# Kernel tuning notes

Measured on AMD Instinct MI355X. Metric: run time of the kernel, lower is better.

The kernel has to match this reference:

```python
import jax, jax.numpy as jnp
import numpy as np

H = W = 64
C = 256
NUM_HEADS = 8

# Static index maps from AbsolutePositionalWeighting.__init__
_center_h = (H - 1) // 2
_center_w = (W - 1) // 2
_gi, _gj = np.meshgrid(np.arange(H), np.arange(W), indexing='ij')
_dx = _gi - _center_h
_dy = _gj - _center_w
DH = max(int(np.abs(_dx).max()), _center_h)
DW = max(int(np.abs(_dy).max()), _center_w)
DX_IDX = jnp.asarray(_dx + DH)  # (H, W)
DY_IDX = jnp.asarray(_dy + DW)  # (H, W)


def setup_inputs() -> dict:
    key = jax.random.key(0)
    ks = jax.random.split(key, 6)
    B, N = 16, H * W
    x1 = jax.random.normal(ks[0], (B, N, C), dtype=jnp.float32)
    x2 = jax.random.normal(ks[1], (B, N, C), dtype=jnp.float32)
    x3 = jax.random.normal(ks[2], (B, N, C), dtype=jnp.float32)
    pos_weights = 0.1 * jax.random.normal(ks[3], (2 * DH + 1, 2 * DW + 1, C), dtype=jnp.float32)
    lepe_w = 0.1 * jax.random.normal(ks[4], (C, 1, 3, 3), dtype=jnp.float32)  # depthwise OIHW
    lepe_b = 0.01 * jax.random.normal(ks[5], (C,), dtype=jnp.float32)
    return {"x1": x1, "x2": x2, "x3": x3, "pos_weights": pos_weights,
            "lepe_w": lepe_w, "lepe_b": lepe_b}


def reference(x1, x2, x3, pos_weights, lepe_w, lepe_b):
    b, n, c = x1.shape
    nh, hd = NUM_HEADS, c // NUM_HEADS

    q = jax.nn.elu(x1) + 1.0
    k = jax.nn.elu(x2) + 1.0
    v = x3

    # Positional gating: sigmoid(pos_weights gathered at per-pixel offsets) -> (N, C)
    pw = jax.nn.sigmoid(pos_weights[DX_IDX, DY_IDX, :]).reshape(n, c)
    q_rope = q * pw[None]  # (b, n, c)
    k_rope = k * pw[None]

    # Split heads: (b, n, nh, hd)
    q4 = q.reshape(b, n, nh, hd)
    k4 = k.reshape(b, n, nh, hd)
    v4 = v.reshape(b, n, nh, hd)
    qr4 = q_rope.reshape(b, n, nh, hd)
    kr4 = k_rope.reshape(b, n, nh, hd)

    # Normalizer z = 1 / (q . mean_n(k) + eps)
    k_mean = k4.mean(axis=1)  # (b, nh, hd)
    z = 1.0 / (jnp.einsum('bnhd,bhd->bnh', q4, k_mean) + 1e-6)

    # Linear attention: kv = (k_rope/sqrt(n))^T (v/sqrt(n)); out = q_rope @ kv * z
    kv = jnp.einsum('bnhd,bnhe->bhde', kr4, v4) / n  # (b, nh, hd, hd)
    attn = jnp.einsum('bnhd,bhde->bnhe', qr4, kv) * z[..., None]
    attn = attn.reshape(b, n, c)

    # LePE: depthwise 3x3 conv on v image (NCHW)
    v_img = v.reshape(b, H, W, c).transpose(0, 3, 1, 2)
    lepe = jax.lax.conv_general_dilated(
        v_img, lepe_w, window_strides=(1, 1), padding='SAME',
        feature_group_count=c,
        dimension_numbers=('NCHW', 'OIHW', 'NCHW'))
    lepe = lepe + lepe_b[None, :, None, None]
    lepe = lepe.transpose(0, 2, 3, 1).reshape(b, n, c)

    return attn + lepe
```

## Files before the change

kernel.cpp:

```cpp
#include <hip/hip_runtime.h>

#define BB 16
#define HIMG 64
#define WIMG 64
#define CC 256
#define NHEAD 8
#define HD 32
#define NN 4096
#define PWD 65
#define PADC 264

typedef short bf16x8 __attribute__((ext_vector_type(8)));
typedef float f32x4 __attribute__((ext_vector_type(4)));

__device__ __forceinline__ float elu1(float x) {
    return x > 0.0f ? x + 1.0f : __expf(x);
}
__device__ __forceinline__ float sigm(float x) {
    return 1.0f / (1.0f + __expf(-x));
}
__device__ __forceinline__ unsigned short f2bf(float f) {
    union { float f; unsigned int u; } v; v.f = f;
    unsigned int r = v.u + 0x7FFFu + ((v.u >> 16) & 1u);
    return (unsigned short)(r >> 16);
}

__global__ __launch_bounds__(256) void k0_pw(
    const float* __restrict__ posw, float* __restrict__ pw)
{
    const int gid = blockIdx.x * 256 + threadIdx.x;
    const int n = gid >> 6;
    const int p = gid & 63;
    const int ii = n >> 6, jj = n & 63;
    const float4 v = *(const float4*)(posw + (size_t)((ii + 1) * PWD + (jj + 1)) * CC + p * 4);
    float4 r;
    r.x = sigm(v.x); r.y = sigm(v.y); r.z = sigm(v.z); r.w = sigm(v.w);
    *(float4*)(pw + (size_t)n * CC + p * 4) = r;
}

__global__ __launch_bounds__(256) void k1_partial(
    const float* __restrict__ x2, const float* __restrict__ x3,
    const float* __restrict__ pw, float* __restrict__ pkv,
    float* __restrict__ pksum, int nchl, int rows)
{
    const int blk   = blockIdx.x;
    const int b     = blk >> nchl;
    const int chunk = blk & ((1 << nchl) - 1);
    const int n0    = chunk * rows;
    const int t     = threadIdx.x;
    const int p     = t & 127;
    const int pp    = p - 64;
    const int rbase = t >> 7;

    const int h   = t >> 5;
    const int idx = t & 31;
    const int dt  = idx & 7;
    const int et  = idx >> 3;

    __shared__ float kr_lds[2][4][CC];
    __shared__ float v_lds[2][4][CC];
    __shared__ float ksum_lds[2][CC];

    float acc[4][8];
#pragma unroll
    for (int a = 0; a < 4; ++a)
#pragma unroll
        for (int e = 0; e < 8; ++e) acc[a][e] = 0.0f;
    float ks0 = 0.f, ks1 = 0.f, ks2 = 0.f, ks3 = 0.f;

    const float* x2b = x2 + (size_t)b * NN * CC;
    const float* x3b = x3 + (size_t)b * NN * CC;

    const int nstep = rows >> 2;
    float4 kx[2], pv[2], vx[2];

    {
        const int r0 = n0;
        if (p < 64) {
#pragma unroll
            for (int it = 0; it < 2; ++it) {
                const int n = r0 + rbase + 2 * it;
                kx[it] = *(const float4*)(x2b + (size_t)n * CC + p * 4);
            }
#pragma unroll
            for (int it = 0; it < 2; ++it) {
                const int n = r0 + rbase + 2 * it;
                pv[it] = *(const float4*)(pw + (size_t)n * CC + p * 4);
            }
        } else {
#pragma unroll
            for (int it = 0; it < 2; ++it) {
                const int n = r0 + rbase + 2 * it;
                vx[it] = *(const float4*)(x3b + (size_t)n * CC + pp * 4);
            }
        }
    }

    int buf = 0;
    for (int s = 0; s < nstep; ++s) {
        if (p < 64) {
#pragma unroll
            for (int it = 0; it < 2; ++it) {
                const int row = rbase + 2 * it;
                float4 kk;
                kk.x = elu1(kx[it].x); kk.y = elu1(kx[it].y);
                kk.z = elu1(kx[it].z); kk.w = elu1(kx[it].w);
                float4 kr;
                kr.x = kk.x * pv[it].x; kr.y = kk.y * pv[it].y;
                kr.z = kk.z * pv[it].z; kr.w = kk.w * pv[it].w;
                *(float4*)(&kr_lds[buf][row][p * 4]) = kr;
                ks0 += kk.x; ks1 += kk.y; ks2 += kk.z; ks3 += kk.w;
            }
        } else {
#pragma unroll
            for (int it = 0; it < 2; ++it)
                *(float4*)(&v_lds[buf][rbase + 2 * it][pp * 4]) = vx[it];
        }
        __syncthreads();
        if (s + 1 < nstep) {
            const int r0 = n0 + (s + 1) * 4;
            if (p < 64) {
#pragma unroll
                for (int it = 0; it < 2; ++it) {
                    const int n = r0 + rbase + 2 * it;
                    kx[it] = *(const float4*)(x2b + (size_t)n * CC + p * 4);
                }
#pragma unroll
                for (int it = 0; it < 2; ++it) {
                    const int n = r0 + rbase + 2 * it;
                    pv[it] = *(const float4*)(pw + (size_t)n * CC + p * 4);
                }
            } else {
#pragma unroll
                for (int it = 0; it < 2; ++it) {
                    const int n = r0 + rbase + 2 * it;
                    vx[it] = *(const float4*)(x3b + (size_t)n * CC + pp * 4);
                }
            }
        }
#pragma unroll
        for (int r = 0; r < 4; ++r) {
            const float4 k4 = *(const float4*)(&kr_lds[buf][r][h * HD + dt * 4]);
            const float4 va = *(const float4*)(&v_lds[buf][r][h * HD + et * 8]);
            const float4 vb = *(const float4*)(&v_lds[buf][r][h * HD + et * 8 + 4]);
            const float kd[4] = {k4.x, k4.y, k4.z, k4.w};
            const float ve[8] = {va.x, va.y, va.z, va.w, vb.x, vb.y, vb.z, vb.w};
#pragma unroll
            for (int a = 0; a < 4; ++a)
#pragma unroll
                for (int e = 0; e < 8; ++e)
                    acc[a][e] = fmaf(kd[a], ve[e], acc[a][e]);
        }
        buf ^= 1;
    }

    if (p < 64) {
        ksum_lds[rbase][p * 4 + 0] = ks0;
        ksum_lds[rbase][p * 4 + 1] = ks1;
        ksum_lds[rbase][p * 4 + 2] = ks2;
        ksum_lds[rbase][p * 4 + 3] = ks3;
    }
    __syncthreads();
    pksum[(size_t)blk * CC + t] = ksum_lds[0][t] + ksum_lds[1][t];

    float* dst = pkv + (size_t)blk * (NHEAD * HD * HD);
#pragma unroll
    for (int a = 0; a < 4; ++a)
#pragma unroll
        for (int e = 0; e < 8; ++e)
            dst[h * (HD * HD) + (dt * 4 + a) * HD + (et * 8 + e)] = acc[a][e];
}

__global__ __launch_bounds__(256) void k2_reduce(
    const float* __restrict__ pkv, const float* __restrict__ pksum,
    unsigned short* __restrict__ kvbT, float* __restrict__ kmean, int nch)
{
    const int gid = blockIdx.x * 256 + threadIdx.x;
    const int b = gid >> 13;
    const int o = gid & 8191;
    float s = 0.f;
#pragma unroll 4
    for (int c = 0; c < nch; ++c)
        s += pkv[(size_t)(b * nch + c) * (NHEAD * HD * HD) + o];
    const int hh = o >> 10, d = (o >> 5) & 31, e = o & 31;
    kvbT[(((size_t)b * NHEAD + hh) * HD + e) * HD + d] = f2bf(s * (1.0f / NN));
    if (o < CC) {
        float ss = 0.f;
#pragma unroll 4
        for (int c = 0; c < nch; ++c)
            ss += pksum[(size_t)(b * nch + c) * CC + o];
        kmean[b * CC + o] = ss * (1.0f / NN);
    }
}

__global__ __launch_bounds__(256, 2) void k3_out(
    const float* __restrict__ x1, const float* __restrict__ x3,
    const float* __restrict__ pw, const unsigned short* __restrict__ kvbT,
    const float* __restrict__ kmean, const float* __restrict__ lw,
    const float* __restrict__ lb, float* __restrict__ out)
{
    const int blk  = blockIdx.x;
    const int b    = blk >> 8;
    const int irow = (blk >> 2) & 63;
    const int jq   = blk & 3;
    const int j0   = jq << 4;
    const int t    = threadIdx.x;

    __shared__ unsigned short qr_bf[16 * PADC];
    __shared__ float attn_lds[16][CC];

    float wreg[9];
#pragma unroll
    for (int q = 0; q < 9; ++q) wreg[q] = lw[t * 9 + q];
    const float bias = lb[t];

    {
        const int p    = t & 63;
        const int pixo = t >> 6;
        const float4 km4 = *(const float4*)(kmean + b * CC + p * 4);
        const float* x1b = x1 + ((size_t)b * NN + (size_t)irow * 64 + j0) * CC;
        const float* pwb = pw + ((size_t)irow * 64 + j0) * CC;
        float4 xv[4], pvv[4];
#pragma unroll
        for (int s = 0; s < 4; ++s)
            xv[s] = *(const float4*)(x1b + (size_t)(s * 4 + pixo) * CC + p * 4);
#pragma unroll
        for (int s = 0; s < 4; ++s)
            pvv[s] = *(const float4*)(pwb + (size_t)(s * 4 + pixo) * CC + p * 4);
#pragma unroll
        for (int s = 0; s < 4; ++s) {
            const int pix = s * 4 + pixo;
            float4 q4;
            q4.x = elu1(xv[s].x); q4.y = elu1(xv[s].y);
            q4.z = elu1(xv[s].z); q4.w = elu1(xv[s].w);
            float zp = q4.x * km4.x + q4.y * km4.y + q4.z * km4.z + q4.w * km4.w;
            zp += __shfl_xor(zp, 1);
            zp += __shfl_xor(zp, 2);
            zp += __shfl_xor(zp, 4);
            const float zin = 1.0f / (zp + 1e-6f);
            ushort4 u;
            u.x = f2bf(q4.x * pvv[s].x * zin);
            u.y = f2bf(q4.y * pvv[s].y * zin);
            u.z = f2bf(q4.z * pvv[s].z * zin);
            u.w = f2bf(q4.w * pvv[s].w * zin);
            *(ushort4*)(&qr_bf[pix * PADC + p * 4]) = u;
        }
    }

    const bool hasU = irow > 0, hasD = irow < 63;
    const float* rU = x3 + ((size_t)b * NN + (size_t)(irow - 1) * 64 + j0) * CC + t;
    const float* rM = x3 + ((size_t)b * NN + (size_t)irow * 64 + j0) * CC + t;
    const float* rD = x3 + ((size_t)b * NN + (size_t)(irow + 1) * 64 + j0) * CC + t;

    float cu[2][10], cm[2][10], cd[2][10];
#pragma unroll
    for (int tt = 0; tt < 2; ++tt)
#pragma unroll
        for (int q = 0; q < 10; ++q) {
            const int col = tt * 8 + q - 1;
            const int g   = j0 + col;
            const bool ok = (g >= 0) && (g < 64);
            const long off = (long)col * CC;
            cm[tt][q] = ok ? rM[off] : 0.f;
            cu[tt][q] = (ok && hasU) ? rU[off] : 0.f;
            cd[tt][q] = (ok && hasD) ? rD[off] : 0.f;
        }

    __syncthreads();

    {
        const int w  = t >> 6;
        const int l  = t & 63;
        const int lr = l & 15;
        const int lg = l >> 4;

        bf16x8 af0 = *(const bf16x8*)(&qr_bf[lr * PADC + (w * 2 + 0) * HD + lg * 8]);
        bf16x8 af1 = *(const bf16x8*)(&qr_bf[lr * PADC + (w * 2 + 1) * HD + lg * 8]);

        f32x4 acc[4];
#pragma unroll
        for (int ct = 0; ct < 4; ++ct) {
            const int head = w * 2 + (ct >> 1);
            const int cl   = (ct & 1) * 16 + lr;
            const bf16x8 bf = *(const bf16x8*)(kvbT +
                (((size_t)b * NHEAD + head) * HD + cl) * HD + lg * 8);
            f32x4 z4 = {0.f, 0.f, 0.f, 0.f};
            acc[ct] = __builtin_amdgcn_mfma_f32_16x16x32_bf16(
                (ct < 2) ? af0 : af1, bf, z4, 0, 0, 0);
        }
#pragma unroll
        for (int ct = 0; ct < 4; ++ct) {
            const int c = (w * 2 + (ct >> 1)) * HD + (ct & 1) * 16 + lr;
#pragma unroll
            for (int r = 0; r < 4; ++r)
                attn_lds[lg * 4 + r][c] = acc[ct][r];
        }
    }

    __syncthreads();

    float* ob = out + ((size_t)b * NN + (size_t)irow * 64 + j0) * CC + t;
#pragma unroll
    for (int tt = 0; tt < 2; ++tt) {
#pragma unroll
        for (int q = 0; q < 8; ++q) {
            const int jl = tt * 8 + q;
            float lepe = bias
                + wreg[0] * cu[tt][q] + wreg[1] * cu[tt][q + 1] + wreg[2] * cu[tt][q + 2]
                + wreg[3] * cm[tt][q] + wreg[4] * cm[tt][q + 1] + wreg[5] * cm[tt][q + 2]
                + wreg[6] * cd[tt][q] + wreg[7] * cd[tt][q + 1] + wreg[8] * cd[tt][q + 2];
            __builtin_nontemporal_store(attn_lds[jl][t] + lepe, ob + (long)jl * CC);
        }
    }
}

extern "C" void kernel_launch(void* const* d_in, const int* in_sizes, int n_in,
                              void* d_out, int out_size, void* d_ws, size_t ws_size,
                              hipStream_t stream) {
    const float* x1   = (const float*)d_in[0];
    const float* x2   = (const float*)d_in[1];
    const float* x3   = (const float*)d_in[2];
    const float* posw = (const float*)d_in[3];
    const float* lw   = (const float*)d_in[4];
    const float* lb   = (const float*)d_in[5];
    float* out = (float*)d_out;

    const size_t pw_sz = (size_t)NN * CC;
    const size_t need64 = (pw_sz + (size_t)16 * 64 * 8192 + (size_t)16 * 64 * 256 +
                           (size_t)16 * 256) * sizeof(float) +
                          (size_t)16 * 8192 * sizeof(unsigned short);
    const int nchl = (ws_size >= need64) ? 6 : 5;
    const int nch  = 1 << nchl;
    const int rows = NN >> nchl;

    float* pwb   = (float*)d_ws;
    float* pkv   = pwb + pw_sz;
    float* pksum = pkv + (size_t)16 * nch * 8192;
    float* kmean = pksum + (size_t)16 * nch * 256;
    unsigned short* kvbT = (unsigned short*)(kmean + (size_t)16 * 256);

    k0_pw<<<1024, 256, 0, stream>>>(posw, pwb);
    k1_partial<<<16 * nch, 256, 0, stream>>>(x2, x3, pwb, pkv, pksum, nchl, rows);
    k2_reduce<<<512, 256, 0, stream>>>(pkv, pksum, kvbT, kmean, nch);
    k3_out<<<BB * 256, 256, 0, stream>>>(x1, x3, pwb, kvbT, kmean, lw, lb, out);
}
```

Before: 100.7 us.

## Deepen k1 prefetch pipeline with uniform thread roles and 8-row steps

Rewrites the k1_partial main loop so every thread loads k, pw and v slices itself, replacing the old split between k-loading and v-loading halves. Each step now processes 8 rows instead of 4. Two register buffer sets keep global loads two steps ahead, with a single raw s_barrier per step. It also adds a min-blocks hint of 2 to launch_bounds. The aim is to keep more memory requests in flight and cut barrier overhead in this bandwidth-bound reduction, at the cost of more registers and LDS. It also assumes the step count is even.

```diff
diff --git a/kernel.cpp b/kernel.cpp
--- a/kernel.cpp
+++ b/kernel.cpp
@@ -38,7 +38,54 @@
     *(float4*)(pw + (size_t)n * CC + p * 4) = r;
 }
 
-__global__ __launch_bounds__(256) void k1_partial(
+
+#define K1_ISSUE(sS, kxS, pvS, vxS)                                          \
+    do {                                                                      \
+        const int r0_ = n0 + (sS) * 8;                                        \
+        const int na_ = r0_ + w, nb_ = r0_ + w + 4;                           \
+        kxS[0] = *(const float4*)(x2b + (size_t)na_ * CC + slot * 4);         \
+        kxS[1] = *(const float4*)(x2b + (size_t)nb_ * CC + slot * 4);         \
+        pvS[0] = *(const float4*)(pw  + (size_t)na_ * CC + slot * 4);         \
+        pvS[1] = *(const float4*)(pw  + (size_t)nb_ * CC + slot * 4);         \
+        vxS[0] = *(const float4*)(x3b + (size_t)na_ * CC + slot * 4);         \
+        vxS[1] = *(const float4*)(x3b + (size_t)nb_ * CC + slot * 4);         \
+    } while (0)
+
+#define K1_STEP(sS, kxS, pvS, vxS, bufS)                                      \
+    do {                                                                      \
+        _Pragma("unroll")                                                     \
+        for (int rp_ = 0; rp_ < 2; ++rp_) {                                   \
+            const int row_ = w + rp_ * 4;                                     \
+            float4 kk_;                                                       \
+            kk_.x = elu1(kxS[rp_].x); kk_.y = elu1(kxS[rp_].y);               \
+            kk_.z = elu1(kxS[rp_].z); kk_.w = elu1(kxS[rp_].w);               \
+            ks0 += kk_.x; ks1 += kk_.y; ks2 += kk_.z; ks3 += kk_.w;           \
+            float4 kr_;                                                       \
+            kr_.x = kk_.x * pvS[rp_].x; kr_.y = kk_.y * pvS[rp_].y;           \
+            kr_.z = kk_.z * pvS[rp_].z; kr_.w = kk_.w * pvS[rp_].w;           \
+            *(float4*)(&kr_lds[bufS][row_][slot * 4]) = kr_;                  \
+            *(float4*)(&v_lds[bufS][row_][slot * 4]) = vxS[rp_];              \
+        }                                                                     \
+        asm volatile("s_waitcnt lgkmcnt(0)" ::: "memory");                    \
+        __builtin_amdgcn_s_barrier();                                         \
+        if ((sS) + 2 < nstep) K1_ISSUE((sS) + 2, kxS, pvS, vxS);              \
+        _Pragma("unroll")                                                     \
+        for (int r_ = 0; r_ < 8; ++r_) {                                      \
+            const float4 k4_ = *(const float4*)(&kr_lds[bufS][r_][h * HD + dt * 4]);   \
+            const float4 va_ = *(const float4*)(&v_lds[bufS][r_][h * HD + et * 8]);    \
+            const float4 vb_ = *(const float4*)(&v_lds[bufS][r_][h * HD + et * 8 + 4]);\
+            const float kd_[4] = {k4_.x, k4_.y, k4_.z, k4_.w};                \
+            const float ve_[8] = {va_.x, va_.y, va_.z, va_.w,                 \
+                                  vb_.x, vb_.y, vb_.z, vb_.w};                \
+            _Pragma("unroll")                                                 \
+            for (int a_ = 0; a_ < 4; ++a_)                                    \
+                _Pragma("unroll")                                             \
+                for (int e_ = 0; e_ < 8; ++e_)                                \
+                    acc[a_][e_] = fmaf(kd_[a_], ve_[e_], acc[a_][e_]);        \
+        }                                                                     \
+    } while (0)
+
+__global__ __launch_bounds__(256, 2) void k1_partial(
     const float* __restrict__ x2, const float* __restrict__ x3,
     const float* __restrict__ pw, float* __restrict__ pkv,
     float* __restrict__ pksum, int nchl, int rows)
@@ -48,18 +95,17 @@
     const int chunk = blk & ((1 << nchl) - 1);
     const int n0    = chunk * rows;
     const int t     = threadIdx.x;
-    const int p     = t & 127;
-    const int pp    = p - 64;
-    const int rbase = t >> 7;
+    const int w     = t >> 6;
+    const int slot  = t & 63;
 
     const int h   = t >> 5;
     const int idx = t & 31;
     const int dt  = idx & 7;
     const int et  = idx >> 3;
 
-    __shared__ float kr_lds[2][4][CC];
-    __shared__ float v_lds[2][4][CC];
-    __shared__ float ksum_lds[2][CC];
+    __shared__ float kr_lds[2][8][CC];
+    __shared__ float v_lds[2][8][CC];
+    __shared__ float ksum_lds[4][CC];
 
     float acc[4][8];
 #pragma unroll
@@ -71,97 +117,26 @@
     const float* x2b = x2 + (size_t)b * NN * CC;
     const float* x3b = x3 + (size_t)b * NN * CC;
 
-    const int nstep = rows >> 2;
-    float4 kx[2], pv[2], vx[2];
-
-    {
-        const int r0 = n0;
-        if (p < 64) {
-#pragma unroll
-            for (int it = 0; it < 2; ++it) {
-                const int n = r0 + rbase + 2 * it;
-                kx[it] = *(const float4*)(x2b + (size_t)n * CC + p * 4);
-            }
-#pragma unroll
-            for (int it = 0; it < 2; ++it) {
-                const int n = r0 + rbase + 2 * it;
-                pv[it] = *(const float4*)(pw + (size_t)n * CC + p * 4);
-            }
-        } else {
-#pragma unroll
-            for (int it = 0; it < 2; ++it) {
-                const int n = r0 + rbase + 2 * it;
-                vx[it] = *(const float4*)(x3b + (size_t)n * CC + pp * 4);
-            }
-        }
-    }
-
-    int buf = 0;
-    for (int s = 0; s < nstep; ++s) {
-        if (p < 64) {
-#pragma unroll
-            for (int it = 0; it < 2; ++it) {
-                const int row = rbase + 2 * it;
-                float4 kk;
-                kk.x = elu1(kx[it].x); kk.y = elu1(kx[it].y);
-                kk.z = elu1(kx[it].z); kk.w = elu1(kx[it].w);
-                float4 kr;
-                kr.x = kk.x * pv[it].x; kr.y = kk.y * pv[it].y;
-                kr.z = kk.z * pv[it].z; kr.w = kk.w * pv[it].w;
-                *(float4*)(&kr_lds[buf][row][p * 4]) = kr;
-                ks0 += kk.x; ks1 += kk.y; ks2 += kk.z; ks3 += kk.w;
-            }
-        } else {
-#pragma unroll
-            for (int it = 0; it < 2; ++it)
-                *(float4*)(&v_lds[buf][rbase + 2 * it][pp * 4]) = vx[it];
-        }
-        __syncthreads();
-        if (s + 1 < nstep) {
-            const int r0 = n0 + (s + 1) * 4;
-            if (p < 64) {
-#pragma unroll
-                for (int it = 0; it < 2; ++it) {
-                    const int n = r0 + rbase + 2 * it;
-                    kx[it] = *(const float4*)(x2b + (size_t)n * CC + p * 4);
-                }
-#pragma unroll
-                for (int it = 0; it < 2; ++it) {
-                    const int n = r0 + rbase + 2 * it;
-                    pv[it] = *(const float4*)(pw + (size_t)n * CC + p * 4);
-                }
-            } else {
-#pragma unroll
-                for (int it = 0; it < 2; ++it) {
-                    const int n = r0 + rbase + 2 * it;
-                    vx[it] = *(const float4*)(x3b + (size_t)n * CC + pp * 4);
-                }
-            }
-        }
-#pragma unroll
-        for (int r = 0; r < 4; ++r) {
-            const float4 k4 = *(const float4*)(&kr_lds[buf][r][h * HD + dt * 4]);
-            const float4 va = *(const float4*)(&v_lds[buf][r][h * HD + et * 8]);
-            const float4 vb = *(const float4*)(&v_lds[buf][r][h * HD + et * 8 + 4]);
-            const float kd[4] = {k4.x, k4.y, k4.z, k4.w};
-            const float ve[8] = {va.x, va.y, va.z, va.w, vb.x, vb.y, vb.z, vb.w};
-#pragma unroll
-            for (int a = 0; a < 4; ++a)
-#pragma unroll
-                for (int e = 0; e < 8; ++e)
-                    acc[a][e] = fmaf(kd[a], ve[e], acc[a][e]);
-        }
-        buf ^= 1;
-    }
-
-    if (p < 64) {
-        ksum_lds[rbase][p * 4 + 0] = ks0;
-        ksum_lds[rbase][p * 4 + 1] = ks1;
-        ksum_lds[rbase][p * 4 + 2] = ks2;
-        ksum_lds[rbase][p * 4 + 3] = ks3;
-    }
+    const int nstep = rows >> 3;
+
+    float4 kx0[2], pv0[2], vx0[2];
+    float4 kx1[2], pv1[2], vx1[2];
+
+    K1_ISSUE(0, kx0, pv0, vx0);
+    K1_ISSUE(1, kx1, pv1, vx1);
+
+    for (int s = 0; s < nstep; s += 2) {
+        K1_STEP(s,     kx0, pv0, vx0, 0);
+        K1_STEP(s + 1, kx1, pv1, vx1, 1);
+    }
+
+    ksum_lds[w][slot * 4 + 0] = ks0;
+    ksum_lds[w][slot * 4 + 1] = ks1;
+    ksum_lds[w][slot * 4 + 2] = ks2;
+    ksum_lds[w][slot * 4 + 3] = ks3;
     __syncthreads();
-    pksum[(size_t)blk * CC + t] = ksum_lds[0][t] + ksum_lds[1][t];
+    pksum[(size_t)blk * CC + t] = ksum_lds[0][t] + ksum_lds[1][t] +
+                                  ksum_lds[2][t] + ksum_lds[3][t];
 
     float* dst = pkv + (size_t)blk * (NHEAD * HD * HD);
 #pragma unroll
```

New measurement: 111.4 us. 1.11x slower.
